# Kernel optimization log

Measured on AMD Instinct MI355X. Metric: run time of the kernel, lower is better.

Reference implementation:

```python
import jax, jax.numpy as jnp
import numpy as np
import math

H = 12  # num heads
EPS = 1e-5


def layer_norm(x, g, b):
    xf = x.astype(jnp.float32)
    mu = jnp.mean(xf, axis=-1, keepdims=True)
    var = jnp.var(xf, axis=-1, keepdims=True)
    return ((xf - mu) * jax.lax.rsqrt(var + EPS) * g + b).astype(x.dtype)


def setup_inputs() -> dict:
    key = jax.random.key(0)
    ks = jax.random.split(key, 8)
    C, M = 768, 3072
    s = 0.02
    inp = {
        "x": jax.random.normal(ks[0], (128, 197, C), dtype=jnp.float32),
        # linear weights stored as [in, out] (y = x @ W + b)
        "Wq": jax.random.normal(ks[1], (C, C), dtype=jnp.float32) * s,
        "bq": jnp.zeros((C,), jnp.float32),
        "Wk": jax.random.normal(ks[2], (C, C), dtype=jnp.float32) * s,
        "bk": jnp.zeros((C,), jnp.float32),
        "Wv": jax.random.normal(ks[3], (C, C), dtype=jnp.float32) * s,
        "bv": jnp.zeros((C,), jnp.float32),
        "Wo": jax.random.normal(ks[4], (C, C), dtype=jnp.float32) * s,
        "bo": jnp.zeros((C,), jnp.float32),
        "W1": jax.random.normal(ks[5], (C, M), dtype=jnp.float32) * s,
        "b1": jnp.zeros((M,), jnp.float32),
        "W2": jax.random.normal(ks[6], (M, C), dtype=jnp.float32) * s,
        "b2": jnp.zeros((C,), jnp.float32),
        "g1": jnp.ones((C,), jnp.float32),
        "beta1": jnp.zeros((C,), jnp.float32),
        "g2": jnp.ones((C,), jnp.float32),
        "beta2": jnp.zeros((C,), jnp.float32),
    }
    return inp


def attention(xn, Wq, bq, Wk, bk, Wv, bv, Wo, bo):
    N, L, C = xn.shape
    Cqk = C // H
    q = (xn @ Wq + bq).reshape(N, L, H, Cqk)
    k = (xn @ Wk + bk).reshape(N, L, H, Cqk)
    v = (xn @ Wv + bv).reshape(N, L, H, Cqk)
    scale = 1.0 / math.sqrt(Cqk)
    aff = jnp.einsum('nqhc,nkhc->nqkh', q * scale, k)  # [N, Lq, Lk, H]
    aff = jax.nn.softmax(aff, axis=-2)                  # softmax over key axis
    mix = jnp.einsum('nqlh,nlhc->nqhc', aff, v)
    return mix.reshape(N, L, C) @ Wo + bo


def reference(x, Wq, bq, Wk, bk, Wv, bv, Wo, bo, W1, b1, W2, b2, g1, beta1, g2, beta2):
    x = x + attention(layer_norm(x, g1, beta1), Wq, bq, Wk, bk, Wv, bv, Wo, bo)
    h = layer_norm(x, g2, beta2) @ W1 + b1
    h = h * jax.nn.sigmoid(1.702 * h)  # QuickGELU
    return x + h @ W2 + b2
```

## Files before the change

kernel.cpp:

```cpp
#include <hip/hip_runtime.h>
#include <hip/hip_bf16.h>

typedef __bf16 bf16_t;
typedef __bf16 bf16x8 __attribute__((ext_vector_type(8)));
typedef float f32x4 __attribute__((ext_vector_type(4)));

#define T_TOK 25216
#define C_DIM 768
#define NH 12
#define LSEQ 197

__device__ __forceinline__ void gload_lds16(const bf16_t* g, bf16_t* l) {
  __builtin_amdgcn_global_load_lds(
      (const __attribute__((address_space(1))) unsigned int*)g,
      (__attribute__((address_space(3))) unsigned int*)l, 16, 0, 0);
}

__global__ void wtrans_k(const float* __restrict__ W, bf16_t* __restrict__ Wt,
                         int K, int N) {
  __shared__ float tile[32][33];
  const int tx = threadIdx.x, ty = threadIdx.y;
  const int bx = blockIdx.x, by = blockIdx.y;
#pragma unroll
  for (int i = ty; i < 32; i += 8)
    tile[i][tx] = W[(long)(by * 32 + i) * N + bx * 32 + tx];
  __syncthreads();
#pragma unroll
  for (int i = ty; i < 32; i += 8)
    Wt[(long)(bx * 32 + i) * K + by * 32 + tx] = (bf16_t)tile[tx][i];
}

__global__ void cat3_k(const float* __restrict__ a, const float* __restrict__ b,
                       const float* __restrict__ c, float* __restrict__ o) {
  int i = blockIdx.x * 256 + threadIdx.x;
  if (i < 2304) o[i] = i < 768 ? a[i] : (i < 1536 ? b[i - 768] : c[i - 1536]);
}

__global__ __launch_bounds__(256) void ln_k(const float* __restrict__ x,
                                            const float* __restrict__ g,
                                            const float* __restrict__ b,
                                            bf16_t* __restrict__ o) {
  const int lane = threadIdx.x & 63;
  const long row = (long)blockIdx.x * 4 + (threadIdx.x >> 6);
  const float* xr = x + row * C_DIM;
  float4 v[3];
  float s = 0.f, sq = 0.f;
#pragma unroll
  for (int i = 0; i < 3; ++i) {
    v[i] = *(const float4*)&xr[i * 256 + lane * 4];
    s += v[i].x + v[i].y + v[i].z + v[i].w;
    sq += v[i].x * v[i].x + v[i].y * v[i].y + v[i].z * v[i].z + v[i].w * v[i].w;
  }
#pragma unroll
  for (int off = 32; off; off >>= 1) {
    s += __shfl_xor(s, off);
    sq += __shfl_xor(sq, off);
  }
  const float mu = s * (1.f / 768.f);
  const float rstd = rsqrtf(sq * (1.f / 768.f) - mu * mu + 1e-5f);
  bf16_t* orow = o + row * C_DIM;
#pragma unroll
  for (int i = 0; i < 3; ++i) {
    const int c = i * 256 + lane * 4;
    const float4 gg = *(const float4*)&g[c];
    const float4 bb = *(const float4*)&b[c];
    bf16_t t4[4];
    t4[0] = (bf16_t)((v[i].x - mu) * rstd * gg.x + bb.x);
    t4[1] = (bf16_t)((v[i].y - mu) * rstd * gg.y + bb.y);
    t4[2] = (bf16_t)((v[i].z - mu) * rstd * gg.z + bb.z);
    t4[3] = (bf16_t)((v[i].w - mu) * rstd * gg.w + bb.w);
    __builtin_memcpy(&orow[c], t4, 8);
  }
}

template <int EPI>
__global__ __launch_bounds__(256) void gemm_bt(
    const bf16_t* __restrict__ A, const bf16_t* __restrict__ Bt,
    const float* __restrict__ bias, const float* __restrict__ res,
    void* __restrict__ outp, int K, int N) {
  __shared__ __align__(16) bf16_t lA[128 * 64];
  __shared__ __align__(16) bf16_t lB[128 * 64];
  const int tid = threadIdx.x;
  const int wave = tid >> 6, lane = tid & 63;
  const int fr = lane & 15, fq = lane >> 4;
  const long rowBase = (long)blockIdx.y * 128;
  const long colBase = (long)blockIdx.x * 128;
  const int wr = (wave >> 1) * 64, wc = (wave & 1) * 64;

  f32x4 acc[4][4];
#pragma unroll
  for (int m = 0; m < 4; ++m)
#pragma unroll
    for (int n = 0; n < 4; ++n) acc[m][n] = (f32x4){0.f, 0.f, 0.f, 0.f};

  const int srow = lane >> 3;
  const int scol = (lane & 7) * 8;
  const int kTiles = K >> 6;
  for (int kt = 0; kt < kTiles; ++kt) {
    const long k0 = (long)kt * 64;
#pragma unroll
    for (int c = 0; c < 4; ++c) {
      const int g = wave * 4 + c;
      gload_lds16(A + (rowBase + 8 * g + srow) * K + k0 + scol, lA + g * 512);
      gload_lds16(Bt + (colBase + 8 * g + srow) * K + k0 + scol, lB + g * 512);
    }
    __syncthreads();
#pragma unroll
    for (int kf = 0; kf < 2; ++kf) {
      bf16x8 af[4], bfr[4];
#pragma unroll
      for (int m = 0; m < 4; ++m)
        af[m] = *(const bf16x8*)&lA[(wr + m * 16 + fr) * 64 + kf * 32 + fq * 8];
#pragma unroll
      for (int n = 0; n < 4; ++n)
        bfr[n] = *(const bf16x8*)&lB[(wc + n * 16 + fr) * 64 + kf * 32 + fq * 8];
#pragma unroll
      for (int m = 0; m < 4; ++m)
#pragma unroll
        for (int n = 0; n < 4; ++n)
          acc[m][n] = __builtin_amdgcn_mfma_f32_16x16x32_bf16(af[m], bfr[n],
                                                              acc[m][n], 0, 0, 0);
    }
    __syncthreads();
  }

#pragma unroll
  for (int m = 0; m < 4; ++m) {
    const long row0 = rowBase + wr + m * 16 + fq * 4;
#pragma unroll
    for (int n = 0; n < 4; ++n) {
      const long col = colBase + wc + n * 16 + fr;
      const float bb = bias[col];
#pragma unroll
      for (int r = 0; r < 4; ++r) {
        const long idx = (row0 + r) * N + col;
        float v = acc[m][n][r] + bb;
        if (EPI == 0) {
          ((bf16_t*)outp)[idx] = (bf16_t)v;
        } else if (EPI == 1) {
          ((float*)outp)[idx] = v + res[idx];
        } else {
          v = v / (1.f + __expf(-1.702f * v));
          ((bf16_t*)outp)[idx] = (bf16_t)v;
        }
      }
    }
  }
}

__global__ __launch_bounds__(256) void attn_k(const bf16_t* __restrict__ qkv,
                                              bf16_t* __restrict__ mix) {
  constexpr int KR = 72;
  constexpr int VR = 232;
  __shared__ __align__(16) bf16_t smem[208 * KR + 64 * VR + 64 * VR];
  bf16_t* lK = smem;
  bf16_t* lVt = smem + 208 * KR;
  bf16_t* lP = lVt + 64 * VR;

  const int tid = threadIdx.x;
  const int wave = tid >> 6, lane = tid & 63;
  const int fr = lane & 15, fq = lane >> 4;
  const int nh = blockIdx.x;
  const int n = nh / NH, h = nh % NH;
  const long t0 = (long)n * LSEQ;
  const long qs = 2304;

  {
    int4 z = {0, 0, 0, 0};
    int4* p = (int4*)smem;
    const int tot = (208 * KR + 2 * 64 * VR) * 2 / 16;
    for (int i = tid; i < tot; i += 256) p[i] = z;
  }
  __syncthreads();

  for (int it = tid; it < 197 * 8; it += 256) {
    int r = it >> 3, cg = it & 7;
    int4 v = *(const int4*)(qkv + (t0 + r) * qs + 768 + h * 64 + cg * 8);
    *(int4*)&lK[r * KR + cg * 8] = v;
  }
  for (int it = tid; it < 197 * 8; it += 256) {
    int r = it >> 3, cg = it & 7;
    int4 v = *(const int4*)(qkv + (t0 + r) * qs + 1536 + h * 64 + cg * 8);
    const bf16_t* pv = (const bf16_t*)&v;
#pragma unroll
    for (int j = 0; j < 8; ++j) lVt[(cg * 8 + j) * VR + r] = pv[j];
  }
  __syncthreads();

  bf16_t* lPw = lP + wave * 16 * VR;

  for (int fi = 0; fi < 4; ++fi) {
    const int f = wave + fi * 4;
    if (f >= 13) break;
    const int qrow = f * 16 + fr;
    const long tq = t0 + (qrow < LSEQ ? qrow : LSEQ - 1);
    const bf16_t* qp = qkv + tq * qs + h * 64;
    bf16x8 a0 = *(const bf16x8*)(qp + fq * 8);
    bf16x8 a1 = *(const bf16x8*)(qp + 32 + fq * 8);

    f32x4 s[13];
#pragma unroll
    for (int j = 0; j < 13; ++j) s[j] = (f32x4){0.f, 0.f, 0.f, 0.f};
#pragma unroll
    for (int j = 0; j < 13; ++j) {
      bf16x8 b0 = *(const bf16x8*)&lK[(j * 16 + fr) * KR + fq * 8];
      s[j] = __builtin_amdgcn_mfma_f32_16x16x32_bf16(a0, b0, s[j], 0, 0, 0);
      bf16x8 b1 = *(const bf16x8*)&lK[(j * 16 + fr) * KR + 32 + fq * 8];
      s[j] = __builtin_amdgcn_mfma_f32_16x16x32_bf16(a1, b1, s[j], 0, 0, 0);
    }
    float mx[4] = {-3e38f, -3e38f, -3e38f, -3e38f};
#pragma unroll
    for (int j = 0; j < 13; ++j) {
      const bool valid = (j * 16 + fr) < LSEQ;
#pragma unroll
      for (int r = 0; r < 4; ++r) {
        float v = s[j][r] * 0.125f;
        v = valid ? v : -3e38f;
        s[j][r] = v;
        mx[r] = fmaxf(mx[r], v);
      }
    }
#pragma unroll
    for (int r = 0; r < 4; ++r) {
      mx[r] = fmaxf(mx[r], __shfl_xor(mx[r], 1));
      mx[r] = fmaxf(mx[r], __shfl_xor(mx[r], 2));
      mx[r] = fmaxf(mx[r], __shfl_xor(mx[r], 4));
      mx[r] = fmaxf(mx[r], __shfl_xor(mx[r], 8));
    }
    float sm[4] = {0.f, 0.f, 0.f, 0.f};
#pragma unroll
    for (int j = 0; j < 13; ++j)
#pragma unroll
      for (int r = 0; r < 4; ++r) {
        float e = __expf(s[j][r] - mx[r]);
        s[j][r] = e;
        sm[r] += e;
      }
#pragma unroll
    for (int r = 0; r < 4; ++r) {
      sm[r] += __shfl_xor(sm[r], 1);
      sm[r] += __shfl_xor(sm[r], 2);
      sm[r] += __shfl_xor(sm[r], 4);
      sm[r] += __shfl_xor(sm[r], 8);
      sm[r] = 1.f / sm[r];
    }
#pragma unroll
    for (int j = 0; j < 13; ++j)
#pragma unroll
      for (int r = 0; r < 4; ++r)
        lPw[(fq * 4 + r) * VR + j * 16 + fr] = (bf16_t)(s[j][r] * sm[r]);
    asm volatile("s_waitcnt lgkmcnt(0)" ::: "memory");

    f32x4 o4[4];
#pragma unroll
    for (int c = 0; c < 4; ++c) o4[c] = (f32x4){0.f, 0.f, 0.f, 0.f};
#pragma unroll
    for (int kc = 0; kc < 7; ++kc) {
      bf16x8 pa = *(const bf16x8*)&lPw[fr * VR + kc * 32 + fq * 8];
#pragma unroll
      for (int c = 0; c < 4; ++c) {
        bf16x8 bv = *(const bf16x8*)&lVt[(c * 16 + fr) * VR + kc * 32 + fq * 8];
        o4[c] = __builtin_amdgcn_mfma_f32_16x16x32_bf16(pa, bv, o4[c], 0, 0, 0);
      }
    }
#pragma unroll
    for (int c = 0; c < 4; ++c)
#pragma unroll
      for (int r = 0; r < 4; ++r) {
        const int q = f * 16 + fq * 4 + r;
        if (q < LSEQ)
          mix[(t0 + q) * C_DIM + h * 64 + c * 16 + fr] = (bf16_t)o4[c][r];
      }
  }
}

extern "C" void kernel_launch(void* const* d_in, const int* in_sizes, int n_in,
                              void* d_out, int out_size, void* d_ws,
                              size_t ws_size, hipStream_t stream) {
  const float* x = (const float*)d_in[0];
  const float* Wq = (const float*)d_in[1];
  const float* bq = (const float*)d_in[2];
  const float* Wk = (const float*)d_in[3];
  const float* bk = (const float*)d_in[4];
  const float* Wv = (const float*)d_in[5];
  const float* bv = (const float*)d_in[6];
  const float* Wo = (const float*)d_in[7];
  const float* bo = (const float*)d_in[8];
  const float* W1 = (const float*)d_in[9];
  const float* b1 = (const float*)d_in[10];
  const float* W2 = (const float*)d_in[11];
  const float* b2 = (const float*)d_in[12];
  const float* g1 = (const float*)d_in[13];
  const float* be1 = (const float*)d_in[14];
  const float* g2 = (const float*)d_in[15];
  const float* be2 = (const float*)d_in[16];

  char* ws = (char*)d_ws;
  size_t off = 0;
  auto alloc = [&](size_t bytes) {
    char* p = ws + off;
    off += (bytes + 255) & ~(size_t)255;
    return p;
  };
  bf16_t* xn = (bf16_t*)alloc((size_t)T_TOK * 768 * 2);
  char* qm = alloc((size_t)T_TOK * 3072 * 2);
  bf16_t* qkv = (bf16_t*)qm;
  bf16_t* mixb = (bf16_t*)(qm + (size_t)T_TOK * 2304 * 2);
  bf16_t* h = (bf16_t*)qm;
  bf16_t* Wqkvt = (bf16_t*)alloc((size_t)2304 * 768 * 2);
  bf16_t* Wot = (bf16_t*)alloc((size_t)768 * 768 * 2);
  bf16_t* W1t = (bf16_t*)alloc((size_t)3072 * 768 * 2);
  bf16_t* W2t = (bf16_t*)alloc((size_t)768 * 3072 * 2);
  float* bqkv = (float*)alloc(2304 * 4);
  float* x2 = (float*)d_out;

  dim3 tb(32, 8);
  wtrans_k<<<dim3(24, 24), tb, 0, stream>>>(Wq, Wqkvt, 768, 768);
  wtrans_k<<<dim3(24, 24), tb, 0, stream>>>(Wk, Wqkvt + 768 * 768, 768, 768);
  wtrans_k<<<dim3(24, 24), tb, 0, stream>>>(Wv, Wqkvt + 2 * 768 * 768, 768, 768);
  wtrans_k<<<dim3(24, 24), tb, 0, stream>>>(Wo, Wot, 768, 768);
  wtrans_k<<<dim3(96, 24), tb, 0, stream>>>(W1, W1t, 768, 3072);
  wtrans_k<<<dim3(24, 96), tb, 0, stream>>>(W2, W2t, 3072, 768);
  cat3_k<<<9, 256, 0, stream>>>(bq, bk, bv, bqkv);

  ln_k<<<T_TOK / 4, 256, 0, stream>>>(x, g1, be1, xn);
  gemm_bt<0><<<dim3(2304 / 128, T_TOK / 128), 256, 0, stream>>>(
      xn, Wqkvt, bqkv, nullptr, qkv, 768, 2304);
  attn_k<<<128 * NH, 256, 0, stream>>>(qkv, mixb);
  gemm_bt<1><<<dim3(768 / 128, T_TOK / 128), 256, 0, stream>>>(
      mixb, Wot, bo, x, x2, 768, 768);
  ln_k<<<T_TOK / 4, 256, 0, stream>>>(x2, g2, be2, xn);
  gemm_bt<2><<<dim3(3072 / 128, T_TOK / 128), 256, 0, stream>>>(
      xn, W1t, b1, nullptr, h, 768, 3072);
  gemm_bt<1><<<dim3(768 / 128, T_TOK / 128), 256, 0, stream>>>(
      h, W2t, b2, x2, (float*)d_out, 3072, 768);
}
```

Before: 861.1 us.

## Replace GEMM with 256x128 triple-buffered 8-wave kernel with swizzled LDS

Replaces the 128x128, 4-wave GEMM with a 256x128-tile, 512-thread kernel. It triple-buffers LDS so global-to-LDS loads for tile t+2 are issued while MFMAs run on tile t, and syncs with vmcnt waits plus a single barrier per k-tile. It also XOR-swizzles LDS columns to cut bank conflicts, remaps block IDs across the XCDs for cache locality, and raises wave priority around the MFMA bursts. The cost is roughly 147KB of LDS per block, which limits occupancy to one block per CU. The last row tile is partial, so loads read past the end of the A rows and the stores are guarded by M.

```diff
diff --git a/kernel.cpp b/kernel.cpp
--- a/kernel.cpp
+++ b/kernel.cpp
@@ -14,6 +14,17 @@
   __builtin_amdgcn_global_load_lds(
       (const __attribute__((address_space(1))) unsigned int*)g,
       (__attribute__((address_space(3))) unsigned int*)l, 16, 0, 0);
+}
+
+template <int N>
+__device__ __forceinline__ void vm_wait() {
+  asm volatile("s_waitcnt vmcnt(%0)" ::"n"(N) : "memory");
+}
+__device__ __forceinline__ void block_bar() {
+  __builtin_amdgcn_sched_barrier(0);
+  asm volatile("" ::: "memory");
+  __builtin_amdgcn_s_barrier();
+  __builtin_amdgcn_sched_barrier(0);
 }
 
 __global__ void wtrans_k(const float* __restrict__ W, bf16_t* __restrict__ Wt,
@@ -74,18 +85,31 @@
 }
 
 template <int EPI>
-__global__ __launch_bounds__(256) void gemm_bt(
+__global__ __launch_bounds__(512) void gemm8(
     const bf16_t* __restrict__ A, const bf16_t* __restrict__ Bt,
     const float* __restrict__ bias, const float* __restrict__ res,
-    void* __restrict__ outp, int K, int N) {
-  __shared__ __align__(16) bf16_t lA[128 * 64];
-  __shared__ __align__(16) bf16_t lB[128 * 64];
+    void* __restrict__ outp, int K, int N, int M) {
+  constexpr int BM = 256, BN = 128, BK = 64;
+  constexpr int AE = BM * BK;
+  constexpr int BUFE = AE + BN * BK;
+  __shared__ __align__(16) bf16_t smem[3][BUFE];
   const int tid = threadIdx.x;
   const int wave = tid >> 6, lane = tid & 63;
   const int fr = lane & 15, fq = lane >> 4;
-  const long rowBase = (long)blockIdx.y * 128;
-  const long colBase = (long)blockIdx.x * 128;
-  const int wr = (wave >> 1) * 64, wc = (wave & 1) * 64;
+
+  const int gx = gridDim.x;
+  const int nwg = gridDim.x * gridDim.y;
+  int bid = blockIdx.y * gx + blockIdx.x;
+  {
+    const int q = nwg >> 3, r = nwg & 7;
+    const int xcd = bid & 7, idx = bid >> 3;
+    bid = (xcd < r ? xcd * (q + 1) : r * (q + 1) + (xcd - r) * q) + idx;
+  }
+  const int bx = bid % gx, by = bid / gx;
+  const long rowBase = (long)by * BM;
+  const long colBase = (long)bx * BN;
+  const int wrow = (wave >> 1) * 64;
+  const int wcol = (wave & 1) * 64;
 
   f32x4 acc[4][4];
 #pragma unroll
@@ -93,55 +117,92 @@
 #pragma unroll
     for (int n = 0; n < 4; ++n) acc[m][n] = (f32x4){0.f, 0.f, 0.f, 0.f};
 
-  const int srow = lane >> 3;
-  const int scol = (lane & 7) * 8;
-  const int kTiles = K >> 6;
-  for (int kt = 0; kt < kTiles; ++kt) {
-    const long k0 = (long)kt * 64;
-#pragma unroll
-    for (int c = 0; c < 4; ++c) {
-      const int g = wave * 4 + c;
-      gload_lds16(A + (rowBase + 8 * g + srow) * K + k0 + scol, lA + g * 512);
-      gload_lds16(Bt + (colBase + 8 * g + srow) * K + k0 + scol, lB + g * 512);
-    }
-    __syncthreads();
+  const int sr = lane >> 3;
+  const int sc = ((lane & 7) ^ sr) * 8;
+  const int arow = wave * 8 + sr;
+  const bf16_t* aP[4];
+  const bf16_t* bP[2];
+#pragma unroll
+  for (int r = 0; r < 4; ++r)
+    aP[r] = A + (rowBase + r * 64 + arow) * (long)K + sc;
+#pragma unroll
+  for (int r = 0; r < 2; ++r)
+    bP[r] = Bt + (colBase + r * 64 + arow) * (long)K + sc;
+
+  auto stage = [&](bf16_t* buf, int t) {
+    const int koff = t * BK;
+#pragma unroll
+    for (int r = 0; r < 4; ++r)
+      gload_lds16(aP[r] + koff, buf + (r * 64 + wave * 8) * BK);
+#pragma unroll
+    for (int r = 0; r < 2; ++r)
+      gload_lds16(bP[r] + koff, buf + AE + (r * 64 + wave * 8) * BK);
+  };
+
+  const int kT = K >> 6;
+
+  auto ktile = [&](const bf16_t* cbuf, bf16_t* nbuf, int t) {
+    if (t == kT - 1) {
+      vm_wait<0>();
+    } else {
+      vm_wait<6>();
+    }
+    block_bar();
 #pragma unroll
     for (int kf = 0; kf < 2; ++kf) {
-      bf16x8 af[4], bfr[4];
+      bf16x8 af[4], bfv[4];
+#pragma unroll
+      for (int m = 0; m < 4; ++m) {
+        const int row = wrow + m * 16 + fr;
+        af[m] = *(const bf16x8*)&cbuf[row * BK + (((kf * 4 + fq) ^ (fr & 7)) * 8)];
+      }
+#pragma unroll
+      for (int n = 0; n < 4; ++n) {
+        const int row = wcol + n * 16 + fr;
+        bfv[n] =
+            *(const bf16x8*)&cbuf[AE + row * BK + (((kf * 4 + fq) ^ (fr & 7)) * 8)];
+      }
+      if (kf == 0 && t + 2 < kT) stage(nbuf, t + 2);
+      __builtin_amdgcn_s_setprio(1);
 #pragma unroll
       for (int m = 0; m < 4; ++m)
-        af[m] = *(const bf16x8*)&lA[(wr + m * 16 + fr) * 64 + kf * 32 + fq * 8];
-#pragma unroll
-      for (int n = 0; n < 4; ++n)
-        bfr[n] = *(const bf16x8*)&lB[(wc + n * 16 + fr) * 64 + kf * 32 + fq * 8];
-#pragma unroll
-      for (int m = 0; m < 4; ++m)
 #pragma unroll
         for (int n = 0; n < 4; ++n)
-          acc[m][n] = __builtin_amdgcn_mfma_f32_16x16x32_bf16(af[m], bfr[n],
+          acc[m][n] = __builtin_amdgcn_mfma_f32_16x16x32_bf16(af[m], bfv[n],
                                                               acc[m][n], 0, 0, 0);
-    }
-    __syncthreads();
+      __builtin_amdgcn_s_setprio(0);
+    }
+  };
+
+  stage(&smem[0][0], 0);
+  stage(&smem[1][0], 1);
+  for (int t = 0; t < kT; t += 3) {
+    ktile(&smem[0][0], &smem[2][0], t);
+    ktile(&smem[1][0], &smem[0][0], t + 1);
+    ktile(&smem[2][0], &smem[1][0], t + 2);
   }
 
 #pragma unroll
   for (int m = 0; m < 4; ++m) {
-    const long row0 = rowBase + wr + m * 16 + fq * 4;
+    const long row0 = rowBase + wrow + m * 16 + fq * 4;
 #pragma unroll
     for (int n = 0; n < 4; ++n) {
-      const long col = colBase + wc + n * 16 + fr;
+      const long col = colBase + wcol + n * 16 + fr;
       const float bb = bias[col];
 #pragma unroll
       for (int r = 0; r < 4; ++r) {
-        const long idx = (row0 + r) * N + col;
-        float v = acc[m][n][r] + bb;
-        if (EPI == 0) {
-          ((bf16_t*)outp)[idx] = (bf16_t)v;
-        } else if (EPI == 1) {
-          ((float*)outp)[idx] = v + res[idx];
-        } else {
-          v = v / (1.f + __expf(-1.702f * v));
-          ((bf16_t*)outp)[idx] = (bf16_t)v;
+        const long rr = row0 + r;
+        if (rr < M) {
+          const long idx = rr * N + col;
+          float v = acc[m][n][r] + bb;
+          if (EPI == 0) {
+            ((bf16_t*)outp)[idx] = (bf16_t)v;
+          } else if (EPI == 1) {
+            ((float*)outp)[idx] = v + res[idx];
+          } else {
+            v = v / (1.f + __expf(-1.702f * v));
+            ((bf16_t*)outp)[idx] = (bf16_t)v;
+          }
         }
       }
     }
@@ -314,6 +375,8 @@
   float* bqkv = (float*)alloc(2304 * 4);
   float* x2 = (float*)d_out;
 
+  const int MT = (T_TOK + 255) / 256;
+
   dim3 tb(32, 8);
   wtrans_k<<<dim3(24, 24), tb, 0, stream>>>(Wq, Wqkvt, 768, 768);
   wtrans_k<<<dim3(24, 24), tb, 0, stream>>>(Wk, Wqkvt + 768 * 768, 768, 768);
@@ -324,14 +387,15 @@
   cat3_k<<<9, 256, 0, stream>>>(bq, bk, bv, bqkv);
 
   ln_k<<<T_TOK / 4, 256, 0, stream>>>(x, g1, be1, xn);
-  gemm_bt<0><<<dim3(2304 / 128, T_TOK / 128), 256, 0, stream>>>(
-      xn, Wqkvt, bqkv, nullptr, qkv, 768, 2304);
+  gemm8<0><<<dim3(2304 / 128, MT), 512, 0, stream>>>(xn, Wqkvt, bqkv, nullptr,
+                                                     qkv, 768, 2304, T_TOK);
   attn_k<<<128 * NH, 256, 0, stream>>>(qkv, mixb);
-  gemm_bt<1><<<dim3(768 / 128, T_TOK / 128), 256, 0, stream>>>(
-      mixb, Wot, bo, x, x2, 768, 768);
+  gemm8<1><<<dim3(768 / 128, MT), 512, 0, stream>>>(mixb, Wot, bo, x, x2, 768,
+                                                    768, T_TOK);
   ln_k<<<T_TOK / 4, 256, 0, stream>>>(x2, g2, be2, xn);
-  gemm_bt<2><<<dim3(3072 / 128, T_TOK / 128), 256, 0, stream>>>(
-      xn, W1t, b1, nullptr, h, 768, 3072);
-  gemm_bt<1><<<dim3(768 / 128, T_TOK / 128), 256, 0, stream>>>(
-      h, W2t, b2, x2, (float*)d_out, 3072, 768);
-}
+  gemm8<2><<<dim3(3072 / 128, MT), 512, 0, stream>>>(xn, W1t, b1, nullptr, h,
+                                                     768, 3072, T_TOK);
+  gemm8<1><<<dim3(768 / 128, MT), 512, 0, stream>>>(h, W2t, b2, x2,
+                                                    (float*)d_out, 3072, 768,
+                                                    T_TOK);
+}
```

Measured after the change: 882.6 us. +2.5%, slower.
